# Kernel optimization log

Measured on AMD Instinct MI355X. Metric: run time of the kernel, lower is better.

Reference implementation:

```python
import jax, jax.numpy as jnp
import numpy as np


def sparsemax(z, axis=0):
    # Standard sparsemax projection onto the simplex (Martins & Astudillo 2016).
    n = z.shape[axis]
    # shift by max for numerical stability (invariant for sparsemax)
    z = z - jnp.max(z, axis=axis, keepdims=True)
    z_sorted = -jnp.sort(-z, axis=axis)  # descending sort along axis
    z_cumsum = jnp.cumsum(z_sorted, axis=axis)
    k_shape = [1] * z.ndim
    k_shape[axis] = n
    k = jnp.arange(1, n + 1, dtype=z.dtype).reshape(k_shape)
    support = (1.0 + k * z_sorted) > z_cumsum  # in-support mask
    k_sup = jnp.sum(support, axis=axis, keepdims=True)  # support size (int)
    # cumsum value at index k_sup-1 along axis
    cs_k = jnp.take_along_axis(z_cumsum, k_sup - 1, axis=axis)
    tau = (cs_k - 1.0) / k_sup.astype(z.dtype)
    return jnp.maximum(z - tau, 0.0)


def setup_inputs() -> dict:
    key = jax.random.key(0)
    k_x, k_a = jax.random.split(key)
    x = jax.random.normal(k_x, (4096, 8192), dtype=jnp.float32)
    a = jnp.asarray(1.0, dtype=jnp.float32)  # nn.Parameter initialized to 1.0
    return {"x": x, "a": a}


def reference(x, a):
    z = -jnp.exp(a) * x
    return sparsemax(z, axis=0)
```

## Files before the change

### kernel.cpp

```cpp
#include <hip/hip_runtime.h>
#include <math.h>


constexpr int ROWS = 4096;
constexpr int COLS = 8192;

constexpr int CB   = 256;
constexpr int RB   = 64;
constexpr int T1   = 512;
constexpr int RPT  = RB / 8;
constexpr int CAPC = 192;

__global__ __launch_bounds__(T1, 4)
void k1_maxfilter(const float* __restrict__ x, const float* __restrict__ a,
                  int* __restrict__ cnt, float2* __restrict__ cand)
{
    __shared__ float smax[8][CB];
    __shared__ float thrS[CB];

    const int tid = threadIdx.x;
    const int l   = tid & 63;
    const int sub = tid >> 6;

    const int  colb = blockIdx.x * CB;
    const int  row0 = blockIdx.y * RB + sub * RPT;
    const long base = (long)row0 * COLS + colb + 4 * l;
    const float s   = -expf(a[0]);

    float z[RPT][4];
#pragma unroll
    for (int k = 0; k < RPT; ++k) {
        const float4 v = *reinterpret_cast<const float4*>(x + base + (long)k * COLS);
        z[k][0] = s * v.x; z[k][1] = s * v.y;
        z[k][2] = s * v.z; z[k][3] = s * v.w;
    }

    float pm[4] = {z[0][0], z[0][1], z[0][2], z[0][3]};
#pragma unroll
    for (int k = 1; k < RPT; ++k)
#pragma unroll
        for (int c = 0; c < 4; ++c) pm[c] = fmaxf(pm[c], z[k][c]);
#pragma unroll
    for (int c = 0; c < 4; ++c) smax[sub][4 * l + c] = pm[c];
    __syncthreads();
    if (tid < CB) {
        float m = smax[0][tid];
#pragma unroll
        for (int w = 1; w < 8; ++w) m = fmaxf(m, smax[w][tid]);
        thrS[tid] = m - 1.0f;
    }
    __syncthreads();

    const float t0 = thrS[4 * l + 0];
    const float t1 = thrS[4 * l + 1];
    const float t2 = thrS[4 * l + 2];
    const float t3 = thrS[4 * l + 3];
    const int c0 = colb + 4 * l;
#pragma unroll
    for (int k = 0; k < RPT; ++k) {
        const int row = row0 + k;
        const float fr = __int_as_float(row);
        if (z[k][0] > t0) { int i = atomicAdd(&cnt[c0 + 0], 1);
            if (i < CAPC) cand[(long)(c0 + 0) * CAPC + i] = make_float2(z[k][0], fr); }
        if (z[k][1] > t1) { int i = atomicAdd(&cnt[c0 + 1], 1);
            if (i < CAPC) cand[(long)(c0 + 1) * CAPC + i] = make_float2(z[k][1], fr); }
        if (z[k][2] > t2) { int i = atomicAdd(&cnt[c0 + 2], 1);
            if (i < CAPC) cand[(long)(c0 + 2) * CAPC + i] = make_float2(z[k][2], fr); }
        if (z[k][3] > t3) { int i = atomicAdd(&cnt[c0 + 3], 1);
            if (i < CAPC) cand[(long)(c0 + 3) * CAPC + i] = make_float2(z[k][3], fr); }
    }
}

__global__ __launch_bounds__(256, 4)
void k2_solve_scatter(const int* __restrict__ cnt, const float2* __restrict__ cand,
                      const float* __restrict__ x, const float* __restrict__ a,
                      float* __restrict__ out)
{
    const int lane = threadIdx.x & 63;
    const int wv   = threadIdx.x >> 6;
    const int col  = blockIdx.x * 4 + wv;
    const int K    = cnt[col];

    if (K <= CAPC) {
        const int s0 = lane, s1 = lane + 64, s2 = lane + 128;
        float v0 = -3.3e38f, v1 = -3.3e38f, v2 = -3.3e38f;
        int   r0 = 0, r1 = 0, r2 = 0;
        const long cbase = (long)col * CAPC;
        if (s0 < K) { float2 p = cand[cbase + s0]; v0 = p.x; r0 = __float_as_int(p.y); }
        if (s1 < K) { float2 p = cand[cbase + s1]; v1 = p.x; r1 = __float_as_int(p.y); }
        if (s2 < K) { float2 p = cand[cbase + s2]; v2 = p.x; r2 = __float_as_int(p.y); }

        float t = -3.0e38f, prev = 0.f;
        for (int it = 0; it < CAPC + 4; ++it) {
            float ss = 0.f, sc = 0.f;
            if (v0 > t) { ss += v0; sc += 1.f; }
            if (v1 > t) { ss += v1; sc += 1.f; }
            if (v2 > t) { ss += v2; sc += 1.f; }
#pragma unroll
            for (int m = 1; m < 64; m <<= 1) {
                ss += __shfl_xor(ss, m, 64);
                sc += __shfl_xor(sc, m, 64);
            }
            t = (ss - 1.0f) / sc;
            if (sc == prev) break;
            prev = sc;
        }
        if (v0 > t) out[(long)r0 * COLS + col] = v0 - t;
        if (v1 > t) out[(long)r1 * COLS + col] = v1 - t;
        if (v2 > t) out[(long)r2 * COLS + col] = v2 - t;
    } else {
        const float s = -expf(a[0]);
        float t = -3.0e38f, prev = 0.f;
        for (int it = 0; it < 256; ++it) {
            float ss = 0.f, sc = 0.f;
            for (int i = 0; i < ROWS / 64; ++i) {
                const float zz = s * x[(long)(lane + i * 64) * COLS + col];
                if (zz > t) { ss += zz; sc += 1.f; }
            }
#pragma unroll
            for (int m = 1; m < 64; m <<= 1) {
                ss += __shfl_xor(ss, m, 64);
                sc += __shfl_xor(sc, m, 64);
            }
            t = (ss - 1.0f) / sc;
            if (sc == prev) break;
            prev = sc;
        }
        for (int i = 0; i < ROWS / 64; ++i) {
            const long r = lane + i * 64;
            const float zz = s * x[r * COLS + col];
            if (zz > t) out[r * COLS + col] = zz - t;
        }
    }
}

extern "C" void kernel_launch(void* const* d_in, const int* in_sizes, int n_in,
                              void* d_out, int out_size, void* d_ws, size_t ws_size,
                              hipStream_t stream) {
    const float* x = (const float*)d_in[0];
    const float* a = (const float*)d_in[1];
    float* out = (float*)d_out;

    char*   ws   = (char*)d_ws;
    int*    cnt  = (int*)ws;
    float2* cand = (float2*)(ws + 64 * 1024);

    hipMemsetAsync(cnt, 0, COLS * sizeof(int), stream);
    hipMemsetAsync(out, 0, (size_t)ROWS * COLS * sizeof(float), stream);
    hipLaunchKernelGGL(k1_maxfilter, dim3(COLS / CB, ROWS / RB), dim3(T1), 0, stream,
                       x, a, cnt, cand);
    hipLaunchKernelGGL(k2_solve_scatter, dim3(COLS / 4), dim3(256), 0, stream,
                       cnt, cand, x, a, out);
}
```

Baseline: 315.1 us.

## Filter candidates with a global column threshold via separate min-reduction passes

Replaces the block-local max filter with a two-pass global column minimum (row-panel partial mins, then a reduction) that gives an exact per-column threshold (max-1) in x space. A separate filter kernel reads x again, compares against the LDS-resident thresholds, and atomically appends far fewer candidates into padded per-column counters. The solve then handles at most 64 candidates per column with one value per lane. This reads x twice instead of once and adds kernels and a partial-min buffer. In exchange it should cut atomic traffic, contention and candidate writes, and shrink the solve loop.

```diff
diff --git a/kernel.cpp b/kernel.cpp
--- a/kernel.cpp
+++ b/kernel.cpp
@@ -4,98 +4,128 @@
 
 constexpr int ROWS = 4096;
 constexpr int COLS = 8192;
+constexpr int CAPC = 64;
+constexpr int CPAD = 16;
 
-constexpr int CB   = 256;
-constexpr int RB   = 64;
-constexpr int T1   = 512;
-constexpr int RPT  = RB / 8;
-constexpr int CAPC = 192;
+constexpr int PANA = 16;
+constexpr int NPA  = ROWS / PANA;
+constexpr int PANC = 8;
 
-__global__ __launch_bounds__(T1, 4)
-void k1_maxfilter(const float* __restrict__ x, const float* __restrict__ a,
-                  int* __restrict__ cnt, float2* __restrict__ cand)
+__global__ __launch_bounds__(1024)
+void k_pmax(const float* __restrict__ x, float* __restrict__ pminx)
 {
-    __shared__ float smax[8][CB];
-    __shared__ float thrS[CB];
+    const int t = threadIdx.x;
+    const int b = blockIdx.x;
+    const long row0 = (long)b * PANA;
 
-    const int tid = threadIdx.x;
-    const int l   = tid & 63;
-    const int sub = tid >> 6;
+    float m[2][4];
+#pragma unroll
+    for (int ch = 0; ch < 2; ++ch)
+#pragma unroll
+        for (int j = 0; j < 4; ++j) m[ch][j] = 3.0e38f;
 
-    const int  colb = blockIdx.x * CB;
-    const int  row0 = blockIdx.y * RB + sub * RPT;
-    const long base = (long)row0 * COLS + colb + 4 * l;
+    for (int r = 0; r < PANA; ++r) {
+        const long rb = (row0 + r) * COLS;
+#pragma unroll
+        for (int ch = 0; ch < 2; ++ch) {
+            const int col = ch * 4096 + t * 4;
+            const float4 v = *reinterpret_cast<const float4*>(x + rb + col);
+            m[ch][0] = fminf(m[ch][0], v.x);
+            m[ch][1] = fminf(m[ch][1], v.y);
+            m[ch][2] = fminf(m[ch][2], v.z);
+            m[ch][3] = fminf(m[ch][3], v.w);
+        }
+    }
+#pragma unroll
+    for (int ch = 0; ch < 2; ++ch) {
+        float4 o = make_float4(m[ch][0], m[ch][1], m[ch][2], m[ch][3]);
+        *reinterpret_cast<float4*>(pminx + (long)b * COLS + ch * 4096 + t * 4) = o;
+    }
+}
+
+__global__ __launch_bounds__(256)
+void k_reduce(const float* __restrict__ pminx, const float* __restrict__ a,
+              float* __restrict__ thrx)
+{
+    __shared__ float red[8][33];
+    const int t  = threadIdx.x;
+    const int c  = t & 31;
+    const int sl = t >> 5;
+    const int col = blockIdx.x * 32 + c;
+
+    float m = 3.0e38f;
+    for (int p = sl * 32; p < sl * 32 + 32; ++p)
+        m = fminf(m, pminx[(long)p * COLS + col]);
+    red[sl][c] = m;
+    __syncthreads();
+    if (t < 32) {
+        float mm = red[0][t];
+#pragma unroll
+        for (int k = 1; k < 8; ++k) mm = fminf(mm, red[k][t]);
+        const float s = -expf(a[0]);
+        thrx[blockIdx.x * 32 + t] = (s * mm - 1.000002f) / s;
+    }
+}
+
+__global__ __launch_bounds__(512, 2)
+void k_filter(const float* __restrict__ x, const float* __restrict__ a,
+              const float* __restrict__ thrx,
+              int* __restrict__ cnt, float2* __restrict__ cand)
+{
+    __shared__ float tl[COLS];
+    const int t = threadIdx.x;
+    for (int i = t; i < COLS / 4; i += 512)
+        reinterpret_cast<float4*>(tl)[i] =
+            reinterpret_cast<const float4*>(thrx)[i];
+    __syncthreads();
+
+    const long row0 = (long)blockIdx.x * PANC;
     const float s   = -expf(a[0]);
 
-    float z[RPT][4];
+    for (int r = 0; r < PANC; ++r) {
+        const int  row = (int)row0 + r;
+        const long rb  = (long)row * COLS;
 #pragma unroll
-    for (int k = 0; k < RPT; ++k) {
-        const float4 v = *reinterpret_cast<const float4*>(x + base + (long)k * COLS);
-        z[k][0] = s * v.x; z[k][1] = s * v.y;
-        z[k][2] = s * v.z; z[k][3] = s * v.w;
-    }
-
-    float pm[4] = {z[0][0], z[0][1], z[0][2], z[0][3]};
-#pragma unroll
-    for (int k = 1; k < RPT; ++k)
-#pragma unroll
-        for (int c = 0; c < 4; ++c) pm[c] = fmaxf(pm[c], z[k][c]);
-#pragma unroll
-    for (int c = 0; c < 4; ++c) smax[sub][4 * l + c] = pm[c];
-    __syncthreads();
-    if (tid < CB) {
-        float m = smax[0][tid];
-#pragma unroll
-        for (int w = 1; w < 8; ++w) m = fmaxf(m, smax[w][tid]);
-        thrS[tid] = m - 1.0f;
-    }
-    __syncthreads();
-
-    const float t0 = thrS[4 * l + 0];
-    const float t1 = thrS[4 * l + 1];
-    const float t2 = thrS[4 * l + 2];
-    const float t3 = thrS[4 * l + 3];
-    const int c0 = colb + 4 * l;
-#pragma unroll
-    for (int k = 0; k < RPT; ++k) {
-        const int row = row0 + k;
-        const float fr = __int_as_float(row);
-        if (z[k][0] > t0) { int i = atomicAdd(&cnt[c0 + 0], 1);
-            if (i < CAPC) cand[(long)(c0 + 0) * CAPC + i] = make_float2(z[k][0], fr); }
-        if (z[k][1] > t1) { int i = atomicAdd(&cnt[c0 + 1], 1);
-            if (i < CAPC) cand[(long)(c0 + 1) * CAPC + i] = make_float2(z[k][1], fr); }
-        if (z[k][2] > t2) { int i = atomicAdd(&cnt[c0 + 2], 1);
-            if (i < CAPC) cand[(long)(c0 + 2) * CAPC + i] = make_float2(z[k][2], fr); }
-        if (z[k][3] > t3) { int i = atomicAdd(&cnt[c0 + 3], 1);
-            if (i < CAPC) cand[(long)(c0 + 3) * CAPC + i] = make_float2(z[k][3], fr); }
+        for (int ch = 0; ch < 4; ++ch) {
+            const int col = ch * 2048 + t * 4;
+            const float4 v  = *reinterpret_cast<const float4*>(x + rb + col);
+            const float4 th = *reinterpret_cast<const float4*>(tl + col);
+            if (v.x < th.x) { int i = atomicAdd(&cnt[(col + 0) * CPAD], 1);
+                if (i < CAPC) cand[(long)(col + 0) * CAPC + i] =
+                    make_float2(s * v.x, __int_as_float(row)); }
+            if (v.y < th.y) { int i = atomicAdd(&cnt[(col + 1) * CPAD], 1);
+                if (i < CAPC) cand[(long)(col + 1) * CAPC + i] =
+                    make_float2(s * v.y, __int_as_float(row)); }
+            if (v.z < th.z) { int i = atomicAdd(&cnt[(col + 2) * CPAD], 1);
+                if (i < CAPC) cand[(long)(col + 2) * CAPC + i] =
+                    make_float2(s * v.z, __int_as_float(row)); }
+            if (v.w < th.w) { int i = atomicAdd(&cnt[(col + 3) * CPAD], 1);
+                if (i < CAPC) cand[(long)(col + 3) * CAPC + i] =
+                    make_float2(s * v.w, __int_as_float(row)); }
+        }
     }
 }
 
 __global__ __launch_bounds__(256, 4)
-void k2_solve_scatter(const int* __restrict__ cnt, const float2* __restrict__ cand,
-                      const float* __restrict__ x, const float* __restrict__ a,
-                      float* __restrict__ out)
+void k_solve(const int* __restrict__ cnt, const float2* __restrict__ cand,
+             const float* __restrict__ x, const float* __restrict__ a,
+             float* __restrict__ out)
 {
     const int lane = threadIdx.x & 63;
-    const int wv   = threadIdx.x >> 6;
-    const int col  = blockIdx.x * 4 + wv;
-    const int K    = cnt[col];
+    const int col  = blockIdx.x * 4 + (threadIdx.x >> 6);
+    const int K    = cnt[col * CPAD];
 
     if (K <= CAPC) {
-        const int s0 = lane, s1 = lane + 64, s2 = lane + 128;
-        float v0 = -3.3e38f, v1 = -3.3e38f, v2 = -3.3e38f;
-        int   r0 = 0, r1 = 0, r2 = 0;
-        const long cbase = (long)col * CAPC;
-        if (s0 < K) { float2 p = cand[cbase + s0]; v0 = p.x; r0 = __float_as_int(p.y); }
-        if (s1 < K) { float2 p = cand[cbase + s1]; v1 = p.x; r1 = __float_as_int(p.y); }
-        if (s2 < K) { float2 p = cand[cbase + s2]; v2 = p.x; r2 = __float_as_int(p.y); }
-
+        float v = -3.3e38f; int row = 0;
+        if (lane < K) {
+            const float2 p = cand[(long)col * CAPC + lane];
+            v = p.x; row = __float_as_int(p.y);
+        }
         float t = -3.0e38f, prev = 0.f;
         for (int it = 0; it < CAPC + 4; ++it) {
-            float ss = 0.f, sc = 0.f;
-            if (v0 > t) { ss += v0; sc += 1.f; }
-            if (v1 > t) { ss += v1; sc += 1.f; }
-            if (v2 > t) { ss += v2; sc += 1.f; }
+            const bool act = v > t;
+            float ss = act ? v : 0.f;
+            float sc = act ? 1.f : 0.f;
 #pragma unroll
             for (int m = 1; m < 64; m <<= 1) {
                 ss += __shfl_xor(ss, m, 64);
@@ -105,9 +135,7 @@
             if (sc == prev) break;
             prev = sc;
         }
-        if (v0 > t) out[(long)r0 * COLS + col] = v0 - t;
-        if (v1 > t) out[(long)r1 * COLS + col] = v1 - t;
-        if (v2 > t) out[(long)r2 * COLS + col] = v2 - t;
+        if (v > t) out[(long)row * COLS + col] = v - t;
     } else {
         const float s = -expf(a[0]);
         float t = -3.0e38f, prev = 0.f;
@@ -141,14 +169,16 @@
     const float* a = (const float*)d_in[1];
     float* out = (float*)d_out;
 
-    char*   ws   = (char*)d_ws;
-    int*    cnt  = (int*)ws;
-    float2* cand = (float2*)(ws + 64 * 1024);
+    char*   ws    = (char*)d_ws;
+    int*    cnt   = (int*)ws;
+    float*  thrx  = (float*)(ws + 512 * 1024);
+    float*  pminx = (float*)(ws + 1024 * 1024);
+    float2* cand  = (float2*)(ws + 9 * 1024 * 1024);
 
-    hipMemsetAsync(cnt, 0, COLS * sizeof(int), stream);
+    hipMemsetAsync(cnt, 0, COLS * CPAD * sizeof(int), stream);
     hipMemsetAsync(out, 0, (size_t)ROWS * COLS * sizeof(float), stream);
-    hipLaunchKernelGGL(k1_maxfilter, dim3(COLS / CB, ROWS / RB), dim3(T1), 0, stream,
-                       x, a, cnt, cand);
-    hipLaunchKernelGGL(k2_solve_scatter, dim3(COLS / 4), dim3(256), 0, stream,
-                       cnt, cand, x, a, out);
+    hipLaunchKernelGGL(k_pmax,   dim3(NPA),        dim3(1024), 0, stream, x, pminx);
+    hipLaunchKernelGGL(k_reduce, dim3(COLS / 32),  dim3(256),  0, stream, pminx, a, thrx);
+    hipLaunchKernelGGL(k_filter, dim3(ROWS / PANC),dim3(512),  0, stream, x, a, thrx, cnt, cand);
+    hipLaunchKernelGGL(k_solve,  dim3(COLS / 4),   dim3(256),  0, stream, cnt, cand, x, a, out);
 }
```

New measurement: 264.4 us. 1.19x faster.
